# Optimization experiments

Measured on AMD Instinct MI355X. Metric: run time of the kernel, lower is better.

The kernel has to match this reference:

```python
import jax, jax.numpy as jnp
import numpy as np

H = 512          # hidden_size
E = 2 * H        # bidirectional embed dim
NH = 8           # attention heads
HD = E // NH     # head dim = 128
SEQ = 10         # hard-coded seq_len in forward
IN = 512         # input_size
OUT = 256        # output_size


def _gru_dir(gi, Whh, bhh, reverse):
    # gi: [B,S,3H] precomputed input-side gate pre-activations
    if reverse:
        gi = gi[:, ::-1]
    B = gi.shape[0]
    h0 = jnp.zeros((B, H), gi.dtype)

    def step(h, gi_t):
        gh = h @ Whh.T + bhh                      # [B,3H]
        ir, iz, inn = jnp.split(gi_t, 3, axis=-1)
        hr, hz, hn = jnp.split(gh, 3, axis=-1)
        r = jax.nn.sigmoid(ir + hr)
        z = jax.nn.sigmoid(iz + hz)
        n = jnp.tanh(inn + r * hn)
        h_new = (1.0 - z) * n + z * h
        return h_new, h_new

    _, hs = jax.lax.scan(step, h0, jnp.swapaxes(gi, 0, 1))
    hs = jnp.swapaxes(hs, 0, 1)                   # [B,S,H]
    if reverse:
        hs = hs[:, ::-1]
    return hs


def _bi_gru_layer(x_seq, Wih, Whh, bih, bhh):
    # Wih: [2, 3H, in]; dir 0 = forward, dir 1 = backward
    outs = []
    for d, rev in ((0, False), (1, True)):
        gi = jnp.einsum('bsi,gi->bsg', x_seq, Wih[d]) + bih[d]
        outs.append(_gru_dir(gi, Whh[d], bhh[d], rev))
    return jnp.concatenate(outs, axis=-1)         # [B,S,2H]


def _attention(x, in_proj_w, in_proj_b, out_proj_w, out_proj_b):
    B, S, _ = x.shape
    qkv = x @ in_proj_w.T + in_proj_b             # [B,S,3E]
    q, k, v = jnp.split(qkv, 3, axis=-1)
    q = q.reshape(B, S, NH, HD)
    k = k.reshape(B, S, NH, HD)
    v = v.reshape(B, S, NH, HD)
    scores = jnp.einsum('bqhd,bkhd->bhqk', q, k) / jnp.sqrt(jnp.asarray(HD, x.dtype))
    attn = jax.nn.softmax(scores, axis=-1)
    o = jnp.einsum('bhqk,bkhd->bqhd', attn, v).reshape(B, S, E)
    return o @ out_proj_w.T + out_proj_b


def _forward(x, Wp, bp, Wih0, Whh0, bih0, bhh0, Wih1, Whh1, bih1, bhh1,
             in_proj_w, in_proj_b, out_proj_w, out_proj_b, W1, b1, W2, b2):
    x_proj = x @ Wp.T + bp                        # [B,H]
    phases = 2.0 * np.pi * np.arange(SEQ) / SEQ
    cos = jnp.asarray(np.cos(phases), x.dtype)    # [S]
    sin = jnp.asarray(np.sin(phases), x.dtype)
    rolled = jnp.roll(x_proj, shift=1, axis=-1)
    x_seq = (x_proj[:, None, :] * (1.0 + 0.1 * cos[None, :, None])
             + 0.05 * sin[None, :, None] * rolled[:, None, :])  # [B,S,H]
    h1 = _bi_gru_layer(x_seq, Wih0, Whh0, bih0, bhh0)           # [B,S,2H]
    gru_out = _bi_gru_layer(h1, Wih1, Whh1, bih1, bhh1)         # [B,S,2H]
    attn_out = _attention(gru_out, in_proj_w, in_proj_b, out_proj_w, out_proj_b)
    aggregated = jnp.mean(gru_out + attn_out, axis=1)           # [B,2H]
    hid = jnp.tanh(aggregated @ W1.T + b1)                      # [B,128]
    return hid @ W2.T + b2                                      # [B,OUT]


def setup_inputs() -> dict:
    key = jax.random.key(0)
    ks = jax.random.split(key, 24)
    s = 1.0 / np.sqrt(H)
    u = lambda k, shape: jax.random.uniform(k, shape, jnp.float32, -s, s)
    return {
        'x': jax.random.normal(ks[0], (4096, IN), jnp.float32),
        'Wp': u(ks[1], (H, IN)), 'bp': u(ks[2], (H,)),
        'Wih0': u(ks[3], (2, 3 * H, H)), 'Whh0': u(ks[4], (2, 3 * H, H)),
        'bih0': u(ks[5], (2, 3 * H)), 'bhh0': u(ks[6], (2, 3 * H)),
        'Wih1': u(ks[7], (2, 3 * H, 2 * H)), 'Whh1': u(ks[8], (2, 3 * H, H)),
        'bih1': u(ks[9], (2, 3 * H)), 'bhh1': u(ks[10], (2, 3 * H)),
        'in_proj_w': u(ks[11], (3 * E, E)), 'in_proj_b': u(ks[12], (3 * E,)),
        'out_proj_w': u(ks[13], (E, E)), 'out_proj_b': u(ks[14], (E,)),
        'W1': u(ks[15], (128, E)), 'b1': u(ks[16], (128,)),
        'W2': u(ks[17], (OUT, 128)), 'b2': u(ks[18], (OUT,)),
    }


def reference(x, Wp, bp, Wih0, Whh0, bih0, bhh0, Wih1, Whh1, bih1, bhh1,
              in_proj_w, in_proj_b, out_proj_w, out_proj_b, W1, b1, W2, b2):
    return _forward(x, Wp, bp, Wih0, Whh0, bih0, bhh0, Wih1, Whh1, bih1, bhh1,
                    in_proj_w, in_proj_b, out_proj_w, out_proj_b, W1, b1, W2, b2)
```

## Files before the change

### kernel.cpp

```cpp
#include <hip/hip_runtime.h>
#include <math.h>


#define SEQ 10

typedef unsigned short bf16u;
typedef __attribute__((ext_vector_type(8))) short short8v;
typedef __attribute__((ext_vector_type(4))) float f32x4;

__device__ __forceinline__ float b2f(bf16u u) {
    union { unsigned int i; float f; } v; v.i = ((unsigned int)u) << 16; return v.f;
}
__device__ __forceinline__ bf16u f2b(float f) {
    union { float f; unsigned int i; } v; v.f = f;
    unsigned int r = (v.i + 0x7FFFu + ((v.i >> 16) & 1u)) >> 16;
    return (bf16u)r;
}
__device__ __forceinline__ float fast_sigm(float x) { return 1.0f / (1.0f + __expf(-x)); }
__device__ __forceinline__ float fast_tanh(float x) {
    float e = __expf(-2.0f * x);
    return 2.0f / (1.0f + e) - 1.0f;
}

__global__ void zero_kernel(float* __restrict__ p, int n)
{
    int i = blockIdx.x * 256 + threadIdx.x;
    if (i < n) p[i] = 0.0f;
}

__global__ void cvt_f2b(const float* __restrict__ src, bf16u* __restrict__ dst, int n4)
{
    int i = blockIdx.x * 256 + threadIdx.x;
    if (i < n4) {
        float4 v = ((const float4*)src)[i];
        ushort4 u; u.x = f2b(v.x); u.y = f2b(v.y); u.z = f2b(v.z); u.w = f2b(v.w);
        ((ushort4*)dst)[i] = u;
    }
}

template <typename TC>
__global__ __launch_bounds__(256) void gemm_mfma(
    const bf16u* __restrict__ A, long long sAz, int lda,
    const bf16u* __restrict__ W, long long sWz,
    const float* __restrict__ bias, long long sBz,
    TC* __restrict__ C, long long sCz, int ldc,
    int K, int act)
{
    __shared__ bf16u As[128 * 64];
    __shared__ bf16u Ws[128 * 64];

    const int z = blockIdx.z;
    A += (long long)z * sAz;
    W += (long long)z * sWz;
    C += (long long)z * sCz;
    const float* bz = bias ? (bias + (long long)z * sBz) : nullptr;

    const int gx = gridDim.x;
    const int nwg = gx * gridDim.y;
    const int orig = blockIdx.y * gx + blockIdx.x;
    const int q = nwg >> 3, rres = nwg & 7;
    const int xcd = orig & 7, loc = orig >> 3;
    const int wgid = (xcd < rres ? xcd * (q + 1) : rres * (q + 1) + (xcd - rres) * q) + loc;
    const int bm = (wgid / gx) * 128;
    const int bn = (wgid % gx) * 128;

    const int tid = threadIdx.x;
    const int lane = tid & 63;
    const int wave = tid >> 6;
    const int wr = (wave >> 1) * 64;
    const int wc = (wave & 1) * 64;
    const int l15 = lane & 15;
    const int lk8 = (lane >> 4) * 8;

    f32x4 acc[4][4];
#pragma unroll
    for (int i = 0; i < 4; ++i)
#pragma unroll
        for (int j = 0; j < 4; ++j)
#pragma unroll
            for (int r = 0; r < 4; ++r) acc[i][j][r] = 0.0f;

    const int sr = wave * 32 + (lane >> 3);
    const int sc = (lane & 7) * 8;
    const bf16u* Ag = A + (long long)(bm + sr) * lda + sc;
    const bf16u* Wg = W + (long long)(bn + sr) * K + sc;
    bf16u* Al = As + wave * 32 * 64;
    bf16u* Wl = Ws + wave * 32 * 64;

    for (int k0 = 0; k0 < K; k0 += 64) {
#pragma unroll
        for (int p = 0; p < 4; ++p) {
            __builtin_amdgcn_global_load_lds(
                (const __attribute__((address_space(1))) void*)(Ag + k0 + (long long)(8 * p) * lda),
                (__attribute__((address_space(3))) void*)(Al + 8 * p * 64), 16, 0, 0);
            __builtin_amdgcn_global_load_lds(
                (const __attribute__((address_space(1))) void*)(Wg + k0 + (long long)(8 * p) * K),
                (__attribute__((address_space(3))) void*)(Wl + 8 * p * 64), 16, 0, 0);
        }
        __syncthreads();
#pragma unroll
        for (int ks = 0; ks < 2; ++ks) {
            short8v af[4], bfr[4];
#pragma unroll
            for (int i = 0; i < 4; ++i)
                af[i] = *(const short8v*)(As + (wr + i * 16 + l15) * 64 + ks * 32 + lk8);
#pragma unroll
            for (int i = 0; i < 4; ++i)
                bfr[i] = *(const short8v*)(Ws + (wc + i * 16 + l15) * 64 + ks * 32 + lk8);
#pragma unroll
            for (int mi = 0; mi < 4; ++mi)
#pragma unroll
                for (int ni = 0; ni < 4; ++ni)
                    acc[mi][ni] = __builtin_amdgcn_mfma_f32_16x16x32_bf16(
                        af[mi], bfr[ni], acc[mi][ni], 0, 0, 0);
        }
        __syncthreads();
    }

    const int r0 = (lane >> 4) * 4;
#pragma unroll
    for (int mi = 0; mi < 4; ++mi) {
#pragma unroll
        for (int ni = 0; ni < 4; ++ni) {
            const int col = bn + wc + ni * 16 + l15;
            float badd = bz ? bz[col] : 0.0f;
#pragma unroll
            for (int r = 0; r < 4; ++r) {
                const long long row = bm + wr + mi * 16 + r0 + r;
                float v = acc[mi][ni][r] + badd;
                if (act) v = tanhf(v);
                if constexpr (sizeof(TC) == 4) ((float*)C)[row * ldc + col] = v;
                else                           ((bf16u*)C)[row * ldc + col] = f2b(v);
            }
        }
    }
}

template <int LAYER>
__global__ __launch_bounds__(256) void gru_step(
    const bf16u* __restrict__ Hb,
    const bf16u* __restrict__ Whh,
    const float* __restrict__ bhh,
    const bf16u* __restrict__ P0,
    const bf16u* __restrict__ P1,
    const float* __restrict__ bih,
    const bf16u* __restrict__ GIT,
    const float* __restrict__ hprev,
    float* __restrict__ hnext,
    bf16u* __restrict__ hnextb,
    bf16u* __restrict__ hout,
    int t, int CB)
{
    __shared__ bf16u As[64 * 64];
    __shared__ bf16u Ws[96 * 64];

    const int z = blockIdx.z;
    const int bn = blockIdx.x * 32;
    const int bm = blockIdx.y * 64;
    const int tid = threadIdx.x;
    const int lane = tid & 63;
    const int wave = tid >> 6;
    const int wm = wave >> 1;
    const int wn = wave & 1;
    const int l15 = lane & 15;
    const int lk8 = (lane >> 4) * 8;

    const bf16u* hsrc = Hb + (long long)z * CB * 512;
    const bf16u* wsrc = Whh + (long long)z * 1536 * 512;

    f32x4 acc[3][2];
#pragma unroll
    for (int g = 0; g < 3; ++g)
#pragma unroll
        for (int i = 0; i < 2; ++i)
#pragma unroll
            for (int r = 0; r < 4; ++r) acc[g][i][r] = 0.0f;

    const int sc = (lane & 7) * 8;
    const bf16u* Ag = hsrc + (long long)(bm + 16 * wave + (lane >> 3)) * 512 + sc;
    bf16u* Al = As + 16 * wave * 64;

    const bf16u* Wg[3];
#pragma unroll
    for (int p = 0; p < 3; ++p) {
        const int lr = 24 * wave + 8 * p + (lane >> 3);
        const int g = lr >> 5, c = lr & 31;
        Wg[p] = wsrc + (long long)(g * 512 + bn + c) * 512 + sc;
    }
    bf16u* Wl = Ws + 24 * wave * 64;

    for (int k0 = 0; k0 < 512; k0 += 64) {
#pragma unroll
        for (int p = 0; p < 2; ++p)
            __builtin_amdgcn_global_load_lds(
                (const __attribute__((address_space(1))) void*)(Ag + k0 + (long long)(8 * p) * 512),
                (__attribute__((address_space(3))) void*)(Al + 8 * p * 64), 16, 0, 0);
#pragma unroll
        for (int p = 0; p < 3; ++p)
            __builtin_amdgcn_global_load_lds(
                (const __attribute__((address_space(1))) void*)(Wg[p] + k0),
                (__attribute__((address_space(3))) void*)(Wl + 8 * p * 64), 16, 0, 0);
        __syncthreads();
#pragma unroll
        for (int ks = 0; ks < 2; ++ks) {
            short8v af[2], bf[3];
#pragma unroll
            for (int mi = 0; mi < 2; ++mi)
                af[mi] = *(const short8v*)(As + (wm * 32 + mi * 16 + l15) * 64 + ks * 32 + lk8);
#pragma unroll
            for (int g = 0; g < 3; ++g)
                bf[g] = *(const short8v*)(Ws + (g * 32 + wn * 16 + l15) * 64 + ks * 32 + lk8);
#pragma unroll
            for (int g = 0; g < 3; ++g)
#pragma unroll
                for (int mi = 0; mi < 2; ++mi)
                    acc[g][mi] = __builtin_amdgcn_mfma_f32_16x16x32_bf16(
                        af[mi], bf[g], acc[g][mi], 0, 0, 0);
        }
        __syncthreads();
    }

    const int r0 = (lane >> 4) * 4;
    const int s = z ? (SEQ - 1 - t) : t;
    float c0 = 0.0f, c1 = 0.0f;
    if (LAYER == 0) {
        float ph = 0.6283185307179586f * (float)s;
        c0 = 1.0f + 0.1f * cosf(ph);
        c1 = 0.05f * sinf(ph);
    }

    const int j = bn + wn * 16 + l15;
    const float bh0 = bhh[z * 1536 + j];
    const float bh1 = bhh[z * 1536 + 512 + j];
    const float bh2 = bhh[z * 1536 + 1024 + j];
    float bi0 = 0, bi1 = 0, bi2 = 0;
    if (LAYER == 0) {
        bi0 = bih[z * 1536 + j];
        bi1 = bih[z * 1536 + 512 + j];
        bi2 = bih[z * 1536 + 1024 + j];
    }

#pragma unroll
    for (int mi = 0; mi < 2; ++mi) {
#pragma unroll
        for (int rr = 0; rr < 4; ++rr) {
            const int m = bm + wm * 32 + mi * 16 + r0 + rr;
            float gr = acc[0][mi][rr] + bh0;
            float gz = acc[1][mi][rr] + bh1;
            float gn = acc[2][mi][rr] + bh2;
            float ir, iz, inn;
            if (LAYER == 0) {
                const bf16u* p0 = P0 + (long long)m * 3072 + z * 1536 + j;
                const bf16u* p1 = P1 + (long long)m * 3072 + z * 1536 + j;
                ir  = c0 * b2f(p0[0])    + c1 * b2f(p1[0])    + bi0;
                iz  = c0 * b2f(p0[512])  + c1 * b2f(p1[512])  + bi1;
                inn = c0 * b2f(p0[1024]) + c1 * b2f(p1[1024]) + bi2;
            } else {
                const bf16u* gi = GIT + (((long long)z * CB + m) * SEQ + s) * 1536 + j;
                ir = b2f(gi[0]); iz = b2f(gi[512]); inn = b2f(gi[1024]);
            }
            const long long ho = ((long long)z * CB + m) * 512 + j;
            float r  = fast_sigm(ir + gr);
            float zz = fast_sigm(iz + gz);
            float n  = fast_tanh(inn + r * gn);
            float hnew = (1.0f - zz) * n + zz * hprev[ho];
            hnext[ho]  = hnew;
            hnextb[ho] = f2b(hnew);
            hout[((long long)m * SEQ + s) * 1024 + z * 512 + j] = f2b(hnew);
        }
    }
}

__global__ void roll_b(const bf16u* __restrict__ xp, bf16u* __restrict__ rl)
{
    int idx = blockIdx.x * 256 + threadIdx.x;
    int i = idx & 511;
    int b = idx >> 9;
    rl[(size_t)b * 512 + i] = xp[(size_t)b * 512 + ((i + 511) & 511)];
}

__global__ __launch_bounds__(128) void attn_kernel(const bf16u* __restrict__ qkv,
                                                   bf16u* __restrict__ o)
{
    const int bh = blockIdx.x;
    const int h = bh & 7;
    const int bl = bh >> 3;
    const int tid = threadIdx.x;

    __shared__ float Q[SEQ][128], Kx[SEQ][128], V[SEQ][128], Amat[SEQ][SEQ];

    const bf16u* base = qkv + (size_t)bl * SEQ * 3072 + h * 128;
#pragma unroll
    for (int s = 0; s < SEQ; ++s) {
        Q[s][tid]  = b2f(base[s * 3072 + tid]);
        Kx[s][tid] = b2f(base[s * 3072 + 1024 + tid]);
        V[s][tid]  = b2f(base[s * 3072 + 2048 + tid]);
    }
    __syncthreads();

    if (tid < SEQ * SEQ) {
        int q = tid / SEQ, k = tid % SEQ;
        float acc = 0.0f;
#pragma unroll 8
        for (int d0 = 0; d0 < 128; ++d0) acc += Q[q][d0] * Kx[k][d0];
        Amat[q][k] = acc * 0.08838834764831845f;
    }
    __syncthreads();

    if (tid < SEQ) {
        float m = -1e30f;
#pragma unroll
        for (int k = 0; k < SEQ; ++k) m = fmaxf(m, Amat[tid][k]);
        float e[SEQ], ssum = 0.0f;
#pragma unroll
        for (int k = 0; k < SEQ; ++k) { e[k] = expf(Amat[tid][k] - m); ssum += e[k]; }
        float inv = 1.0f / ssum;
#pragma unroll
        for (int k = 0; k < SEQ; ++k) Amat[tid][k] = e[k] * inv;
    }
    __syncthreads();

    bf16u* ob = o + (size_t)bl * SEQ * 1024 + h * 128;
#pragma unroll
    for (int q = 0; q < SEQ; ++q) {
        float acc = 0.0f;
#pragma unroll
        for (int k = 0; k < SEQ; ++k) acc += Amat[q][k] * V[k][tid];
        ob[q * 1024 + tid] = f2b(acc);
    }
}

__global__ void mean_kernel(const bf16u* __restrict__ go, const bf16u* __restrict__ ao,
                            bf16u* __restrict__ agg)
{
    int idx = blockIdx.x * 256 + threadIdx.x;
    int j4 = (idx & 255) * 4;
    int bl = idx >> 8;
    const bf16u* g = go + (size_t)bl * (SEQ * 1024) + j4;
    const bf16u* a = ao + (size_t)bl * (SEQ * 1024) + j4;
    float s0 = 0, s1 = 0, s2 = 0, s3 = 0;
#pragma unroll
    for (int t = 0; t < SEQ; ++t) {
        ushort4 gv = *(const ushort4*)(g + t * 1024);
        ushort4 av = *(const ushort4*)(a + t * 1024);
        s0 += b2f(gv.x) + b2f(av.x);
        s1 += b2f(gv.y) + b2f(av.y);
        s2 += b2f(gv.z) + b2f(av.z);
        s3 += b2f(gv.w) + b2f(av.w);
    }
    ushort4 u; u.x = f2b(0.1f * s0); u.y = f2b(0.1f * s1); u.z = f2b(0.1f * s2); u.w = f2b(0.1f * s3);
    *(ushort4*)(agg + (size_t)bl * 1024 + j4) = u;
}

extern "C" void kernel_launch(void* const* d_in, const int* in_sizes, int n_in,
                              void* d_out, int out_size, void* d_ws, size_t ws_size,
                              hipStream_t stream)
{
    const float* x    = (const float*)d_in[0];
    const float* Wp   = (const float*)d_in[1];
    const float* bp   = (const float*)d_in[2];
    const float* Wih0 = (const float*)d_in[3];
    const float* Whh0 = (const float*)d_in[4];
    const float* bih0 = (const float*)d_in[5];
    const float* bhh0 = (const float*)d_in[6];
    const float* Wih1 = (const float*)d_in[7];
    const float* Whh1 = (const float*)d_in[8];
    const float* bih1 = (const float*)d_in[9];
    const float* bhh1 = (const float*)d_in[10];
    const float* ipw  = (const float*)d_in[11];
    const float* ipb  = (const float*)d_in[12];
    const float* opw  = (const float*)d_in[13];
    const float* opb  = (const float*)d_in[14];
    const float* W1   = (const float*)d_in[15];
    const float* b1   = (const float*)d_in[16];
    const float* W2   = (const float*)d_in[17];
    const float* b2   = (const float*)d_in[18];
    float* out = (float*)d_out;

    const long long WBYTES = 9437184LL;
    int CB = 0;
    for (int c = 4096; c >= 128; c >>= 1)
        if (WBYTES + (long long)c * 114688 <= (long long)ws_size) { CB = c; break; }
    if (CB == 0) return;
    const int CBA = CB / 2;

    bf16u* wreg = (bf16u*)d_ws;
    bf16u* Wpb   = wreg;
    bf16u* Wih0b = wreg + 262144;
    bf16u* Whh0b = wreg + 1835008;
    bf16u* Wih1b = wreg;
    bf16u* Whh1b = wreg + 3145728;
    bf16u* ipwb  = wreg;
    bf16u* opwb  = wreg + 3145728;
    bf16u* W1b   = wreg + 4194304;
    bf16u* W2b   = wreg + 4325376;

    char* A0 = (char*)d_ws + WBYTES;
    bf16u* H1c = (bf16u*)A0;
    bf16u* GOc = (bf16u*)(A0 + 20480LL * CB);
    char*  U   = A0 + 40960LL * CB;
    bf16u* P0    = (bf16u*)U;
    bf16u* P1    = (bf16u*)(U + 6144LL * CB);
    bf16u* XB    = (bf16u*)(U + 12288LL * CB);
    bf16u* XPb   = (bf16u*)(U + 13312LL * CB);
    bf16u* RLb   = (bf16u*)(U + 14336LL * CB);
    bf16u* GIT   = (bf16u*)U;
    char*  HC    = U + 61440LL * CB;
    bf16u* QKV   = (bf16u*)U;
    bf16u* OC    = (bf16u*)(U + 30720LL * CB);
    bf16u* AOC   = (bf16u*)(U + 40960LL * CB);
    bf16u* AGGb  = (bf16u*)(U + 51200LL * CB);
    bf16u* HIDb  = (bf16u*)(U + 53248LL * CB);

    const dim3 blk(256);
    const int MB = CB / 128;

    auto cvt = [&](const float* s, bf16u* d, long long nfloats) {
        int n4 = (int)(nfloats / 4);
        cvt_f2b<<<(n4 + 255) / 256, blk, 0, stream>>>(s, d, n4);
    };

    for (int c0 = 0; c0 < 4096; c0 += CB) {
        cvt(x + (long long)c0 * 512, XB, (long long)CB * 512);
        cvt(Wp,   Wpb,   512LL * 512);
        cvt(Wih0, Wih0b, 2LL * 1536 * 512);
        cvt(Whh0, Whh0b, 2LL * 1536 * 512);

        gemm_mfma<bf16u><<<dim3(4, MB, 1), blk, 0, stream>>>(
            XB, 0, 512, Wpb, 0, bp, 0, XPb, 0, 512, 512, 0);
        roll_b<<<CB * 2, blk, 0, stream>>>(XPb, RLb);
        gemm_mfma<bf16u><<<dim3(24, MB, 2), blk, 0, stream>>>(
            XPb, (long long)CB * 512, 512, Wih0b, 0, nullptr, 0,
            P0, (long long)CB * 3072, 3072, 512, 0);

        zero_kernel<<<CB * 6, blk, 0, stream>>>((float*)HC, CB * 1536);
        for (int t = 0; t < SEQ; ++t) {
            const int rb = t & 1;
            float* hprev  = (float*)(HC + (long long)rb * 6144 * CB);
            bf16u* Hbr    = (bf16u*)(HC + (long long)rb * 6144 * CB + 4096LL * CB);
            float* hnext  = (float*)(HC + (long long)(1 - rb) * 6144 * CB);
            bf16u* hnextb = (bf16u*)(HC + (long long)(1 - rb) * 6144 * CB + 4096LL * CB);
            gru_step<0><<<dim3(16, CB / 64, 2), blk, 0, stream>>>(
                Hbr, Whh0b, bhh0, P0, P1, bih0, nullptr,
                hprev, hnext, hnextb, H1c, t, CB);
        }

        cvt(Wih1, Wih1b, 2LL * 1536 * 1024);
        cvt(Whh1, Whh1b, 2LL * 1536 * 512);
        gemm_mfma<bf16u><<<dim3(12, MB * 10, 2), blk, 0, stream>>>(
            H1c, 0, 1024, Wih1b, 1536LL * 1024, bih1, 1536,
            GIT, (long long)CB * SEQ * 1536, 1536, 1024, 0);

        zero_kernel<<<CB * 6, blk, 0, stream>>>((float*)HC, CB * 1536);
        for (int t = 0; t < SEQ; ++t) {
            const int rb = t & 1;
            float* hprev  = (float*)(HC + (long long)rb * 6144 * CB);
            bf16u* Hbr    = (bf16u*)(HC + (long long)rb * 6144 * CB + 4096LL * CB);
            float* hnext  = (float*)(HC + (long long)(1 - rb) * 6144 * CB);
            bf16u* hnextb = (bf16u*)(HC + (long long)(1 - rb) * 6144 * CB + 4096LL * CB);
            gru_step<1><<<dim3(16, CB / 64, 2), blk, 0, stream>>>(
                Hbr, Whh1b, bhh1, nullptr, nullptr, nullptr, GIT,
                hprev, hnext, hnextb, GOc, t, CB);
        }

        cvt(ipw, ipwb, 3072LL * 1024);
        cvt(opw, opwb, 1024LL * 1024);
        cvt(W1,  W1b,  128LL * 1024);
        cvt(W2,  W2b,  256LL * 128);
        for (int a0 = 0; a0 < CB; a0 += CBA) {
            const bf16u* src = GOc + (long long)a0 * 10240;
            gemm_mfma<bf16u><<<dim3(24, CBA * 10 / 128, 1), blk, 0, stream>>>(
                src, 0, 1024, ipwb, 0, ipb, 0, QKV, 0, 3072, 1024, 0);
            attn_kernel<<<CBA * 8, dim3(128), 0, stream>>>(QKV, OC);
            gemm_mfma<bf16u><<<dim3(8, CBA * 10 / 128, 1), blk, 0, stream>>>(
                OC, 0, 1024, opwb, 0, opb, 0, AOC, 0, 1024, 1024, 0);
            mean_kernel<<<CBA, blk, 0, stream>>>(src, AOC, AGGb + (long long)a0 * 1024);
        }
        gemm_mfma<bf16u><<<dim3(1, MB, 1), blk, 0, stream>>>(
            AGGb, 0, 1024, W1b, 0, b1, 0, HIDb, 0, 128, 1024, 1);
        gemm_mfma<float><<<dim3(2, MB, 1), blk, 0, stream>>>(
            HIDb, 0, 128, W2b, 0, b2, 0, out + (long long)c0 * 256, 0, 256, 128, 0);
    }
}
```

Baseline: 2.426 ms.

## Skip first GRU matmul, widen K tile, batch QKV projection per chunk

At t=0 the hidden state is zero, so a FIRST template variant of the GRU step skips the recurrent matmul and the hprev read, and the zero-fill kernels are removed. The non-first step now stages a 128-wide K slice per iteration, which halves the number of barrier rounds but doubles LDS use. The QKV projection is hoisted out of the attention sub-batch loop into a single GEMM over the whole chunk, with scratch buffers relocated to make room. This trades more LDS per block and a larger QKV buffer for fewer launches and syncs.

```diff
diff --git a/kernel.cpp b/kernel.cpp
--- a/kernel.cpp
+++ b/kernel.cpp
@@ -20,12 +20,6 @@
 __device__ __forceinline__ float fast_tanh(float x) {
     float e = __expf(-2.0f * x);
     return 2.0f / (1.0f + e) - 1.0f;
-}
-
-__global__ void zero_kernel(float* __restrict__ p, int n)
-{
-    int i = blockIdx.x * 256 + threadIdx.x;
-    if (i < n) p[i] = 0.0f;
 }
 
 __global__ void cvt_f2b(const float* __restrict__ src, bf16u* __restrict__ dst, int n4)
@@ -136,7 +130,7 @@
     }
 }
 
-template <int LAYER>
+template <int LAYER, bool FIRST>
 __global__ __launch_bounds__(256) void gru_step(
     const bf16u* __restrict__ Hb,
     const bf16u* __restrict__ Whh,
@@ -151,8 +145,8 @@
     bf16u* __restrict__ hout,
     int t, int CB)
 {
-    __shared__ bf16u As[64 * 64];
-    __shared__ bf16u Ws[96 * 64];
+    __shared__ bf16u As[64 * 128];
+    __shared__ bf16u Ws[96 * 128];
 
     const int z = blockIdx.z;
     const int bn = blockIdx.x * 32;
@@ -165,9 +159,6 @@
     const int l15 = lane & 15;
     const int lk8 = (lane >> 4) * 8;
 
-    const bf16u* hsrc = Hb + (long long)z * CB * 512;
-    const bf16u* wsrc = Whh + (long long)z * 1536 * 512;
-
     f32x4 acc[3][2];
 #pragma unroll
     for (int g = 0; g < 3; ++g)
@@ -176,48 +167,54 @@
 #pragma unroll
             for (int r = 0; r < 4; ++r) acc[g][i][r] = 0.0f;
 
-    const int sc = (lane & 7) * 8;
-    const bf16u* Ag = hsrc + (long long)(bm + 16 * wave + (lane >> 3)) * 512 + sc;
-    bf16u* Al = As + 16 * wave * 64;
-
-    const bf16u* Wg[3];
-#pragma unroll
-    for (int p = 0; p < 3; ++p) {
-        const int lr = 24 * wave + 8 * p + (lane >> 3);
-        const int g = lr >> 5, c = lr & 31;
-        Wg[p] = wsrc + (long long)(g * 512 + bn + c) * 512 + sc;
-    }
-    bf16u* Wl = Ws + 24 * wave * 64;
-
-    for (int k0 = 0; k0 < 512; k0 += 64) {
-#pragma unroll
-        for (int p = 0; p < 2; ++p)
-            __builtin_amdgcn_global_load_lds(
-                (const __attribute__((address_space(1))) void*)(Ag + k0 + (long long)(8 * p) * 512),
-                (__attribute__((address_space(3))) void*)(Al + 8 * p * 64), 16, 0, 0);
-#pragma unroll
-        for (int p = 0; p < 3; ++p)
-            __builtin_amdgcn_global_load_lds(
-                (const __attribute__((address_space(1))) void*)(Wg[p] + k0),
-                (__attribute__((address_space(3))) void*)(Wl + 8 * p * 64), 16, 0, 0);
-        __syncthreads();
-#pragma unroll
-        for (int ks = 0; ks < 2; ++ks) {
-            short8v af[2], bf[3];
-#pragma unroll
-            for (int mi = 0; mi < 2; ++mi)
-                af[mi] = *(const short8v*)(As + (wm * 32 + mi * 16 + l15) * 64 + ks * 32 + lk8);
-#pragma unroll
-            for (int g = 0; g < 3; ++g)
-                bf[g] = *(const short8v*)(Ws + (g * 32 + wn * 16 + l15) * 64 + ks * 32 + lk8);
-#pragma unroll
-            for (int g = 0; g < 3; ++g)
+    if constexpr (!FIRST) {
+        const bf16u* hsrc = Hb + (long long)z * CB * 512;
+        const bf16u* wsrc = Whh + (long long)z * 1536 * 512;
+
+        const int srow = lane >> 4;
+        const int sc = (lane & 15) * 8;
+        const bf16u* Ag = hsrc + (long long)(bm + 16 * wave + srow) * 512 + sc;
+        bf16u* Al = As + (16 * wave) * 128;
+
+        const bf16u* Wg[6];
+#pragma unroll
+        for (int p = 0; p < 6; ++p) {
+            const int lr = 24 * wave + 4 * p + srow;
+            const int g = lr >> 5, c = lr & 31;
+            Wg[p] = wsrc + (long long)(g * 512 + bn + c) * 512 + sc;
+        }
+        bf16u* Wl = Ws + (24 * wave) * 128;
+
+        for (int k0 = 0; k0 < 512; k0 += 128) {
+#pragma unroll
+            for (int p = 0; p < 4; ++p)
+                __builtin_amdgcn_global_load_lds(
+                    (const __attribute__((address_space(1))) void*)(Ag + k0 + (long long)(4 * p) * 512),
+                    (__attribute__((address_space(3))) void*)(Al + (4 * p) * 128), 16, 0, 0);
+#pragma unroll
+            for (int p = 0; p < 6; ++p)
+                __builtin_amdgcn_global_load_lds(
+                    (const __attribute__((address_space(1))) void*)(Wg[p] + k0),
+                    (__attribute__((address_space(3))) void*)(Wl + (4 * p) * 128), 16, 0, 0);
+            __syncthreads();
+#pragma unroll
+            for (int ks = 0; ks < 4; ++ks) {
+                short8v af[2], bf[3];
 #pragma unroll
                 for (int mi = 0; mi < 2; ++mi)
-                    acc[g][mi] = __builtin_amdgcn_mfma_f32_16x16x32_bf16(
-                        af[mi], bf[g], acc[g][mi], 0, 0, 0);
-        }
-        __syncthreads();
+                    af[mi] = *(const short8v*)(As + (wm * 32 + mi * 16 + l15) * 128 + ks * 32 + lk8);
+#pragma unroll
+                for (int g = 0; g < 3; ++g)
+                    bf[g] = *(const short8v*)(Ws + (g * 32 + wn * 16 + l15) * 128 + ks * 32 + lk8);
+#pragma unroll
+                for (int g = 0; g < 3; ++g)
+#pragma unroll
+                    for (int mi = 0; mi < 2; ++mi)
+                        acc[g][mi] = __builtin_amdgcn_mfma_f32_16x16x32_bf16(
+                            af[mi], bf[g], acc[g][mi], 0, 0, 0);
+            }
+            __syncthreads();
+        }
     }
 
     const int r0 = (lane >> 4) * 4;
@@ -263,7 +260,9 @@
             float r  = fast_sigm(ir + gr);
             float zz = fast_sigm(iz + gz);
             float n  = fast_tanh(inn + r * gn);
-            float hnew = (1.0f - zz) * n + zz * hprev[ho];
+            float hnew;
+            if constexpr (FIRST) hnew = (1.0f - zz) * n;
+            else                 hnew = (1.0f - zz) * n + zz * hprev[ho];
             hnext[ho]  = hnew;
             hnextb[ho] = f2b(hnew);
             hout[((long long)m * SEQ + s) * 1024 + z * 512 + j] = f2b(hnew);
@@ -407,10 +406,10 @@
     bf16u* GIT   = (bf16u*)U;
     char*  HC    = U + 61440LL * CB;
     bf16u* QKV   = (bf16u*)U;
-    bf16u* OC    = (bf16u*)(U + 30720LL * CB);
-    bf16u* AOC   = (bf16u*)(U + 40960LL * CB);
-    bf16u* AGGb  = (bf16u*)(U + 51200LL * CB);
-    bf16u* HIDb  = (bf16u*)(U + 53248LL * CB);
+    bf16u* OC    = (bf16u*)(U + 61440LL * CB);
+    bf16u* AOC   = (bf16u*)A0;
+    bf16u* AGGb  = (bf16u*)(A0 + 10240LL * CB);
+    bf16u* HIDb  = (bf16u*)(A0 + 12288LL * CB);
 
     const dim3 blk(256);
     const int MB = CB / 128;
@@ -433,16 +432,20 @@
             XPb, (long long)CB * 512, 512, Wih0b, 0, nullptr, 0,
             P0, (long long)CB * 3072, 3072, 512, 0);
 
-        zero_kernel<<<CB * 6, blk, 0, stream>>>((float*)HC, CB * 1536);
         for (int t = 0; t < SEQ; ++t) {
             const int rb = t & 1;
             float* hprev  = (float*)(HC + (long long)rb * 6144 * CB);
             bf16u* Hbr    = (bf16u*)(HC + (long long)rb * 6144 * CB + 4096LL * CB);
             float* hnext  = (float*)(HC + (long long)(1 - rb) * 6144 * CB);
             bf16u* hnextb = (bf16u*)(HC + (long long)(1 - rb) * 6144 * CB + 4096LL * CB);
-            gru_step<0><<<dim3(16, CB / 64, 2), blk, 0, stream>>>(
-                Hbr, Whh0b, bhh0, P0, P1, bih0, nullptr,
-                hprev, hnext, hnextb, H1c, t, CB);
+            if (t == 0)
+                gru_step<0, true><<<dim3(16, CB / 64, 2), blk, 0, stream>>>(
+                    Hbr, Whh0b, bhh0, P0, P1, bih0, nullptr,
+                    hprev, hnext, hnextb, H1c, t, CB);
+            else
+                gru_step<0, false><<<dim3(16, CB / 64, 2), blk, 0, stream>>>(
+                    Hbr, Whh0b, bhh0, P0, P1, bih0, nullptr,
+                    hprev, hnext, hnextb, H1c, t, CB);
         }
 
         cvt(Wih1, Wih1b, 2LL * 1536 * 1024);
@@ -451,30 +454,35 @@
             H1c, 0, 1024, Wih1b, 1536LL * 1024, bih1, 1536,
             GIT, (long long)CB * SEQ * 1536, 1536, 1024, 0);
 
-        zero_kernel<<<CB * 6, blk, 0, stream>>>((float*)HC, CB * 1536);
         for (int t = 0; t < SEQ; ++t) {
             const int rb = t & 1;
             float* hprev  = (float*)(HC + (long long)rb * 6144 * CB);
             bf16u* Hbr    = (bf16u*)(HC + (long long)rb * 6144 * CB + 4096LL * CB);
             float* hnext  = (float*)(HC + (long long)(1 - rb) * 6144 * CB);
             bf16u* hnextb = (bf16u*)(HC + (long long)(1 - rb) * 6144 * CB + 4096LL * CB);
-            gru_step<1><<<dim3(16, CB / 64, 2), blk, 0, stream>>>(
-                Hbr, Whh1b, bhh1, nullptr, nullptr, nullptr, GIT,
-                hprev, hnext, hnextb, GOc, t, CB);
+            if (t == 0)
+                gru_step<1, true><<<dim3(16, CB / 64, 2), blk, 0, stream>>>(
+                    Hbr, Whh1b, bhh1, nullptr, nullptr, nullptr, GIT,
+                    hprev, hnext, hnextb, GOc, t, CB);
+            else
+                gru_step<1, false><<<dim3(16, CB / 64, 2), blk, 0, stream>>>(
+                    Hbr, Whh1b, bhh1, nullptr, nullptr, nullptr, GIT,
+                    hprev, hnext, hnextb, GOc, t, CB);
         }
 
         cvt(ipw, ipwb, 3072LL * 1024);
         cvt(opw, opwb, 1024LL * 1024);
         cvt(W1,  W1b,  128LL * 1024);
         cvt(W2,  W2b,  256LL * 128);
+        gemm_mfma<bf16u><<<dim3(24, MB * 10, 1), blk, 0, stream>>>(
+            GOc, 0, 1024, ipwb, 0, ipb, 0, QKV, 0, 3072, 1024, 0);
         for (int a0 = 0; a0 < CB; a0 += CBA) {
-            const bf16u* src = GOc + (long long)a0 * 10240;
-            gemm_mfma<bf16u><<<dim3(24, CBA * 10 / 128, 1), blk, 0, stream>>>(
-                src, 0, 1024, ipwb, 0, ipb, 0, QKV, 0, 3072, 1024, 0);
-            attn_kernel<<<CBA * 8, dim3(128), 0, stream>>>(QKV, OC);
+            attn_kernel<<<CBA * 8, dim3(128), 0, stream>>>(
+                QKV + (long long)a0 * 30720, OC);
             gemm_mfma<bf16u><<<dim3(8, CBA * 10 / 128, 1), blk, 0, stream>>>(
                 OC, 0, 1024, opwb, 0, opb, 0, AOC, 0, 1024, 1024, 0);
-            mean_kernel<<<CBA, blk, 0, stream>>>(src, AOC, AGGb + (long long)a0 * 1024);
+            mean_kernel<<<CBA, blk, 0, stream>>>(
+                GOc + (long long)a0 * 10240, AOC, AGGb + (long long)a0 * 1024);
         }
         gemm_mfma<bf16u><<<dim3(1, MB, 1), blk, 0, stream>>>(
             AGGb, 0, 1024, W1b, 0, b1, 0, HIDb, 0, 128, 1024, 1);
```

New measurement: 2.596 ms. 7.0% more time.
